# Kernel optimization log

Measured on AMD Instinct MI355X. Metric: run time of the kernel, lower is better.

The kernel has to match this reference:

```python
import jax, jax.numpy as jnp
import numpy as np

N, L, E, CE = 16384, 50, 64, 128
N_USERS, N_RATINGS, N_CONTENTS = 100000, 6, 50000

def _lin(key, din, dout):
    k1, k2 = jax.random.split(key)
    s = 1.0 / np.sqrt(din)
    return (jax.random.uniform(k1, (din, dout), jnp.float32, -s, s),
            jax.random.uniform(k2, (dout,), jnp.float32, -s, s))

def setup_inputs() -> dict:
    key = jax.random.key(0)
    ks = jax.random.split(key, 16)
    We_w, We_b = _lin(ks[0], CE, E)
    W1_w, W1_b = _lin(ks[1], 2 * E, E)
    W2_w, W2_b = _lin(ks[2], E, E)
    A1_w, A1_b = _lin(ks[3], 2 * E, E)
    A2_w, A2_b = _lin(ks[4], E, E)
    A3_w, A3_b = _lin(ks[5], E, 1)
    Ow_w, Ow_b = _lin(ks[6], 2 * E, E)
    return {
        "u2e": jax.random.normal(ks[7], (N_USERS, E), jnp.float32),
        "r2e": jax.random.normal(ks[8], (N_RATINGS, E), jnp.float32),
        "content_emb": jax.random.normal(ks[9], (N_CONTENTS, CE), jnp.float32),
        "We_w": We_w, "We_b": We_b,
        "W1_w": W1_w, "W1_b": W1_b,
        "W2_w": W2_w, "W2_b": W2_b,
        "A1_w": A1_w, "A1_b": A1_b,
        "A2_w": A2_w, "A2_b": A2_b,
        "A3_w": A3_w, "A3_b": A3_b,
        "Ow_w": Ow_w, "Ow_b": Ow_b,
        "nodes": jnp.arange(N, dtype=jnp.int64) if jax.config.jax_enable_x64 else jnp.arange(N, dtype=jnp.int32),
        "pu_history": jax.random.randint(ks[10], (N, L), 0, N_USERS),
        "pr_history": jax.random.randint(ks[11], (N, L), 0, N_RATINGS),
        "lengths": jax.random.randint(ks[12], (N,), 1, L + 1),
        "pr_content": jax.random.randint(ks[13], (N,), 0, N_CONTENTS),
    }

def reference(u2e, r2e, content_emb, We_w, We_b, W1_w, W1_b, W2_w, W2_b,
              A1_w, A1_b, A2_w, A2_b, A3_w, A3_b, Ow_w, Ow_b,
              nodes, pu_history, pr_history, lengths, pr_content):
    # mask of valid (non-padded) neighbors per node: [N, L]
    mask = jnp.arange(pu_history.shape[1])[None, :] < lengths[:, None]
    # post content representation: [N, E]
    post = jax.nn.relu(content_emb[pr_content] @ We_w + We_b)
    # neighbor embeddings: [N, L, E]
    u = u2e[pu_history]
    r = r2e[pr_history]
    x = jax.nn.relu(jnp.concatenate([u, r], axis=-1) @ W1_w + W1_b)
    o = jax.nn.relu(x @ W2_w + W2_b)  # [N, L, E]
    # attention over variable-length neighbor history
    pr = jnp.broadcast_to(post[:, None, :], o.shape)
    a = jax.nn.relu(jnp.concatenate([o, pr], axis=-1) @ A1_w + A1_b)
    a = jax.nn.relu(a @ A2_w + A2_b)
    logits = (a @ A3_w + A3_b)[..., 0]  # [N, L]
    logits = jnp.where(mask, logits, -jnp.inf)
    att = jax.nn.softmax(logits, axis=1)  # [N, L], padded slots -> 0
    hist = jnp.einsum("nl,nle->ne", att, o)  # [N, E]
    out = jax.nn.relu(jnp.concatenate([hist, post], axis=-1) @ Ow_w + Ow_b)
    return out
```

## Files before the change

### kernel.cpp

```cpp
#include <hip/hip_runtime.h>
#include <hip/hip_bf16.h>
#include <math.h>


#define NN 16384
#define LL 50
#define EE 64
#define NUE 6400000

typedef __attribute__((ext_vector_type(8))) short short8;
typedef __attribute__((ext_vector_type(4))) float f32x4;

static __device__ __forceinline__ unsigned short f2bf(float x) {
  __hip_bfloat16 h = __float2bfloat16(x);
  unsigned short u;
  __builtin_memcpy(&u, &h, 2);
  return u;
}

static __device__ __forceinline__ float bf2f(unsigned short u) {
  unsigned int v = ((unsigned int)u) << 16;
  float f;
  __builtin_memcpy(&f, &v, 4);
  return f;
}

static __device__ __forceinline__ f32x4 ld4(const float* p) {
  return *(const f32x4*)p;
}

static __device__ __forceinline__ f32x4 relu4(f32x4 a) {
  f32x4 r;
  r[0] = fmaxf(a[0], 0.f); r[1] = fmaxf(a[1], 0.f);
  r[2] = fmaxf(a[2], 0.f); r[3] = fmaxf(a[3], 0.f);
  return r;
}

static __device__ __forceinline__ void gl_lds16(const unsigned short* g,
                                                unsigned char* l) {
  __builtin_amdgcn_global_load_lds(
      (const __attribute__((address_space(1))) void*)g,
      (__attribute__((address_space(3))) void*)l, 16, 0, 0);
}

#define MFMA(A, B, C) __builtin_amdgcn_mfma_f32_16x16x32_bf16((A), (B), (C), 0, 0, 0)
#define SWZ(row, byteoff) ((byteoff) ^ (((row) & 7) << 4))

__global__ __launch_bounds__(256)
void conv_kernel(const float* __restrict__ u2e, const float* __restrict__ r2e,
                 unsigned short* __restrict__ ur_bf) {
  const int total8 = (NUE + 384) / 8;
  for (int i = blockIdx.x * 256 + (int)threadIdx.x; i < total8;
       i += gridDim.x * 256) {
    const long long e0 = (long long)i * 8;
    const float* src = (e0 < NUE) ? (u2e + e0) : (r2e + (e0 - NUE));
    float4 a = *(const float4*)src;
    float4 b = *(const float4*)(src + 4);
    short8 v;
    v[0] = (short)f2bf(a.x); v[1] = (short)f2bf(a.y);
    v[2] = (short)f2bf(a.z); v[3] = (short)f2bf(a.w);
    v[4] = (short)f2bf(b.x); v[5] = (short)f2bf(b.y);
    v[6] = (short)f2bf(b.z); v[7] = (short)f2bf(b.w);
    *reinterpret_cast<short8*>(ur_bf + e0) = v;
  }
}

__global__ __launch_bounds__(256)
void setup_kernel(const float* __restrict__ content_emb,
                  const int* __restrict__ pr_content,
                  const float* __restrict__ We_w, const float* __restrict__ We_b,
                  const float* __restrict__ A1_w, const float* __restrict__ A1_b,
                  float* __restrict__ post_ws, float* __restrict__ abase_ws) {
  const int sub = (int)threadIdx.x >> 6;
  const int e = (int)threadIdx.x & 63;
  const int n = blockIdx.x * 4 + sub;
  __shared__ float ce_s[4][128];
  __shared__ float post_s[4][64];
  const float* ce = content_emb + (size_t)pr_content[n] * 128;
  ce_s[sub][e] = ce[e];
  ce_s[sub][64 + e] = ce[64 + e];
  __syncthreads();
  float acc = We_b[e];
#pragma unroll 8
  for (int k = 0; k < 128; ++k) acc = fmaf(ce_s[sub][k], We_w[k * EE + e], acc);
  float po = fmaxf(acc, 0.f);
  post_s[sub][e] = po;
  post_ws[(size_t)n * EE + e] = po;
  __syncthreads();
  float ab = A1_b[e];
#pragma unroll 8
  for (int k = 0; k < 64; ++k)
    ab = fmaf(post_s[sub][k], A1_w[(64 + k) * EE + e], ab);
  abase_ws[(size_t)n * EE + e] = ab;
}

__global__ __launch_bounds__(1024)
void aux_kernel(const int* __restrict__ lengths,
                const float* __restrict__ W1_w, const float* __restrict__ W2_w,
                const float* __restrict__ A1_w, const float* __restrict__ A2_w,
                int* __restrict__ buckets, int* __restrict__ wdesc,
                int* __restrict__ Wout, unsigned short* __restrict__ frag_ws) {
  const int tid = (int)threadIdx.x;
  const int lanei = tid & 63;
  __shared__ int cnt_s[4];
  if (tid < 4) cnt_s[tid] = 0;
  __syncthreads();

  for (int i0 = 0; i0 < NN; i0 += 1024) {
    const int n = i0 + tid;
    const int nt = (lengths[n] + 15) >> 4;
#pragma unroll
    for (int b = 1; b <= 4; ++b) {
      const unsigned long long mask = __ballot(nt == b);
      if (mask) {
        const int leader = __ffsll((long long)mask) - 1;
        int base = 0;
        if (lanei == leader) base = atomicAdd(&cnt_s[b - 1], (int)__popcll(mask));
        base = __shfl(base, leader);
        if (nt == b) {
          const int rank = __popcll(mask & ((1ull << lanei) - 1ull));
          buckets[(b - 1) * NN + base + rank] = n;
        }
      }
    }
  }
  __syncthreads();

  const int c1 = cnt_s[0], c2 = cnt_s[1], c3 = cnt_s[2], c4 = cnt_s[3];
  const int u1 = (c1 < c3) ? c1 : c3;
  const int p2 = c2 >> 1, odd2 = c2 & 1;
  const int rem1 = c1 - u1;
  const int o2ones = odd2 ? ((rem1 < 2) ? rem1 : 2) : 0;
  const int rem1b = rem1 - o2ones;
  const int w4 = c4, w3 = c3, w2 = p2 + odd2, w1 = (rem1b + 3) >> 2;
  const int W = w4 + w3 + w2 + w1;
  if (tid == 0) *Wout = W;

  const int* b1 = buckets;
  const int* b2 = buckets + NN;
  const int* b3 = buckets + 2 * NN;
  const int* b4 = buckets + 3 * NN;
#define ENC(n, t) ((n) | ((t) << 14) | (lengths[(n)] << 16))
  for (int w = tid; w < W; w += 1024) {
    int d0 = -1, d1 = -1, d2 = -1, d3 = -1;
    if (w < w4) {
      const int n = b4[w];
      d0 = ENC(n, 0); d1 = ENC(n, 1); d2 = ENC(n, 2); d3 = ENC(n, 3);
    } else if (w < w4 + w3) {
      const int i = w - w4;
      const int n = b3[i];
      d0 = ENC(n, 0); d1 = ENC(n, 1); d2 = ENC(n, 2);
      if (i < u1) d3 = ENC(b1[i], 0);
    } else if (w < w4 + w3 + w2) {
      const int i = w - w4 - w3;
      if (i < p2) {
        const int a = b2[2 * i], b = b2[2 * i + 1];
        d0 = ENC(a, 0); d1 = ENC(a, 1); d2 = ENC(b, 0); d3 = ENC(b, 1);
      } else {
        const int a = b2[c2 - 1];
        d0 = ENC(a, 0); d1 = ENC(a, 1);
        if (o2ones > 0) d2 = ENC(b1[u1], 0);
        if (o2ones > 1) d3 = ENC(b1[u1 + 1], 0);
      }
    } else {
      const int i = w - w4 - w3 - w2;
      const int basei = u1 + o2ones + 4 * i;
      if (basei + 0 < c1) d0 = ENC(b1[basei + 0], 0);
      if (basei + 1 < c1) d1 = ENC(b1[basei + 1], 0);
      if (basei + 2 < c1) d2 = ENC(b1[basei + 2], 0);
      if (basei + 3 < c1) d3 = ENC(b1[basei + 3], 0);
    }
    int4 v; v.x = d0; v.y = d1; v.z = d2; v.w = d3;
    *(int4*)(wdesc + 4 * w) = v;
  }
#undef ENC

  for (int idx = tid; idx < 2560; idx += 1024) {
    const float* Wm;
    int w, s, lane;
    if (idx < 1024) {
      w = idx >> 8; s = (idx >> 6) & 3; lane = idx & 63; Wm = W1_w;
    } else {
      int r = idx - 1024;
      int li = r >> 9;
      w = (r >> 7) & 3; s = (r >> 6) & 1; lane = r & 63;
      Wm = (li == 0) ? W2_w : (li == 1) ? A1_w : A2_w;
    }
    const int g = lane >> 4, c = lane & 15;
#pragma unroll
    for (int j = 0; j < 8; ++j)
      frag_ws[idx * 8 + j] = f2bf(Wm[(32 * s + 8 * g + j) * EE + 16 * w + c]);
  }
}

__global__
__attribute__((amdgpu_flat_work_group_size(256, 256)))
__attribute__((amdgpu_waves_per_eu(4, 4)))
void fused_kernel(const unsigned short* __restrict__ ur_bf,
                  const float* __restrict__ W1_b, const float* __restrict__ W2_b,
                  const float* __restrict__ A2_b,
                  const float* __restrict__ A3_w, const float* __restrict__ A3_b,
                  const float* __restrict__ Ow_w, const float* __restrict__ Ow_b,
                  const int* __restrict__ pu_history,
                  const int* __restrict__ pr_history,
                  const short8* __restrict__ pf,
                  const float* __restrict__ post_ws,
                  const float* __restrict__ abase_ws,
                  const int* __restrict__ wdesc, const int* __restrict__ Wptr,
                  float* __restrict__ out) {
  const int tid = (int)threadIdx.x;
  const int lane = tid & 63;
  const int w = tid >> 6;
  const int g = lane >> 4;
  const int c = lane & 15;

  __shared__ __align__(16) unsigned char xb0[16384];
  __shared__ __align__(16) unsigned char xb1[8192];
  __shared__ __align__(16) unsigned char xb2[8192];
  __shared__ float bias_s[256];
  __shared__ float lpart[4][64];
  __shared__ float att_s[64];
  __shared__ float h_s[4][128];

  short8 Wf1[4], Wf2[2], Wf3[2], Wf4[2];
#pragma unroll
  for (int s = 0; s < 4; ++s) Wf1[s] = pf[(w * 4 + s) * 64 + lane];
#pragma unroll
  for (int s = 0; s < 2; ++s) {
    Wf2[s] = pf[1024 + (w * 2 + s) * 64 + lane];
    Wf3[s] = pf[1536 + (w * 2 + s) * 64 + lane];
    Wf4[s] = pf[2048 + (w * 2 + s) * 64 + lane];
  }
  if (tid < 64) {
    bias_s[tid]       = W1_b[tid];
    bias_s[64 + tid]  = W2_b[tid];
    bias_s[128 + tid] = A2_b[tid];
    bias_s[192 + tid] = A3_w[tid];
  }

  const float b3 = A3_b[0];
  const float owb = Ow_b[lane];
  const unsigned short* rbase = ur_bf + NUE;
  const int Wtot = *Wptr;
  const int stride = gridDim.x;

  const int r0 = lane >> 4;
  const int cE = (lane & 15) ^ r0;
  const int cO = (lane & 15) ^ (r0 + 4);
  const unsigned short* tabE = ((cE < 8) ? ur_bf : rbase) + (cE & 7) * 8;
  const unsigned short* tabO = ((cO < 8) ? ur_bf : rbase) + (cO & 7) * 8;
  const int* histE = (cE < 8) ? pu_history : pr_history;
  const int* histO = (cO < 8) ? pu_history : pr_history;
  unsigned char* const sbase = xb0 + w * 4096;

  {
    const int dn = wdesc[blockIdx.x * 4 + w];
    if (dn >= 0) {
      const int nd = (dn & 0x3FFF) * LL + (((dn >> 14) & 3) << 4);
      const int ln = (dn >> 16) & 63;
      const int lim = ln - (((dn >> 14) & 3) << 4);
#pragma unroll
      for (int b = 0; b < 4; ++b) {
        const int row = b * 4 + r0;
        const bool vv = row < lim;
        const int* hh = (b & 1) ? histO : histE;
        const unsigned short* tt = (b & 1) ? tabO : tabE;
        if (vv) {
          const int idx = hh[nd + row];
          gl_lds16(tt + (size_t)idx * EE, sbase + b * 1024);
        }
      }
    }
  }
  __syncthreads();

  for (int wi = blockIdx.x; wi < Wtot; wi += stride) {
    const int d0 = wdesc[wi * 4 + 0];
    const int d1 = wdesc[wi * 4 + 1];
    const int d2 = wdesc[wi * 4 + 2];
    const int d3 = wdesc[wi * 4 + 3];

    const int win = wi + stride;
    int sidx0 = 0, sidx1 = 0, sidx2 = 0, sidx3 = 0;
    int svmask = 0;
    if (win < Wtot) {
      const int dn = wdesc[win * 4 + w];
      if (dn >= 0) {
        const int nd = (dn & 0x3FFF) * LL + (((dn >> 14) & 3) << 4);
        const int lim = ((dn >> 16) & 63) - (((dn >> 14) & 3) << 4);
        if (r0 + 0  < lim) { sidx0 = histE[nd + r0];      svmask |= 1; }
        if (r0 + 4  < lim) { sidx1 = histO[nd + r0 + 4];  svmask |= 2; }
        if (r0 + 8  < lim) { sidx2 = histE[nd + r0 + 8];  svmask |= 4; }
        if (r0 + 12 < lim) { sidx3 = histO[nd + r0 + 12]; svmask |= 8; }
      }
    }

    f32x4 acc[4];

    {
      const f32x4 binit = ld4(bias_s + 16 * w + 4 * g);
#pragma unroll
      for (int rt = 0; rt < 4; ++rt) acc[rt] = binit;
#pragma unroll
      for (int s = 0; s < 4; ++s)
#pragma unroll
        for (int rt = 0; rt < 4; ++rt) {
          const int row = rt * 16 + c;
          const short8 bf =
              *(const short8*)(xb0 + SWZ(row, row * 256 + s * 64 + g * 16));
          acc[rt] = MFMA(Wf1[s], bf, acc[rt]);
        }
#pragma unroll
      for (int rt = 0; rt < 4; ++rt) {
        const f32x4 v = relu4(acc[rt]);
        ushort4 p;
        p.x = f2bf(v[0]); p.y = f2bf(v[1]); p.z = f2bf(v[2]); p.w = f2bf(v[3]);
        const int row = rt * 16 + c;
        *(ushort4*)(xb1 + SWZ(row, row * 128 + w * 32 + g * 8)) = p;
      }
    }
    __syncthreads();

    if (svmask & 1) gl_lds16(tabE + (size_t)sidx0 * EE, sbase);
    if (svmask & 2) gl_lds16(tabO + (size_t)sidx1 * EE, sbase + 1024);
    if (svmask & 4) gl_lds16(tabE + (size_t)sidx2 * EE, sbase + 2048);
    if (svmask & 8) gl_lds16(tabO + (size_t)sidx3 * EE, sbase + 3072);

    {
      const f32x4 binit = ld4(bias_s + 64 + 16 * w + 4 * g);
#pragma unroll
      for (int rt = 0; rt < 4; ++rt) acc[rt] = binit;
#pragma unroll
      for (int s = 0; s < 2; ++s)
#pragma unroll
        for (int rt = 0; rt < 4; ++rt) {
          const int row = rt * 16 + c;
          const short8 bf =
              *(const short8*)(xb1 + SWZ(row, row * 128 + s * 64 + g * 16));
          acc[rt] = MFMA(Wf2[s], bf, acc[rt]);
        }
#pragma unroll
      for (int rt = 0; rt < 4; ++rt) {
        const f32x4 v = relu4(acc[rt]);
        ushort4 p;
        p.x = f2bf(v[0]); p.y = f2bf(v[1]); p.z = f2bf(v[2]); p.w = f2bf(v[3]);
        const int row = rt * 16 + c;
        *(ushort4*)(xb2 + SWZ(row, row * 128 + w * 32 + g * 8)) = p;
      }
    }
    __syncthreads();

    {
      {
        const int n0 = (d0 >= 0) ? (d0 & 0x3FFF) : 0;
        const int n1 = (d1 >= 0) ? (d1 & 0x3FFF) : 0;
        const int n2 = (d2 >= 0) ? (d2 & 0x3FFF) : 0;
        const int n3 = (d3 >= 0) ? (d3 & 0x3FFF) : 0;
        acc[0] = ld4(abase_ws + (size_t)n0 * EE + 16 * w + 4 * g);
        acc[1] = ld4(abase_ws + (size_t)n1 * EE + 16 * w + 4 * g);
        acc[2] = ld4(abase_ws + (size_t)n2 * EE + 16 * w + 4 * g);
        acc[3] = ld4(abase_ws + (size_t)n3 * EE + 16 * w + 4 * g);
      }
#pragma unroll
      for (int s = 0; s < 2; ++s)
#pragma unroll
        for (int rt = 0; rt < 4; ++rt) {
          const int row = rt * 16 + c;
          const short8 bf =
              *(const short8*)(xb2 + SWZ(row, row * 128 + s * 64 + g * 16));
          acc[rt] = MFMA(Wf3[s], bf, acc[rt]);
        }
#pragma unroll
      for (int rt = 0; rt < 4; ++rt) {
        const f32x4 v = relu4(acc[rt]);
        ushort4 p;
        p.x = f2bf(v[0]); p.y = f2bf(v[1]); p.z = f2bf(v[2]); p.w = f2bf(v[3]);
        const int row = rt * 16 + c;
        *(ushort4*)(xb1 + SWZ(row, row * 128 + w * 32 + g * 8)) = p;
      }
    }
    __syncthreads();

    {
      const f32x4 binit = ld4(bias_s + 128 + 16 * w + 4 * g);
#pragma unroll
      for (int rt = 0; rt < 4; ++rt) acc[rt] = binit;
#pragma unroll
      for (int s = 0; s < 2; ++s)
#pragma unroll
        for (int rt = 0; rt < 4; ++rt) {
          const int row = rt * 16 + c;
          const short8 bf =
              *(const short8*)(xb1 + SWZ(row, row * 128 + s * 64 + g * 16));
          acc[rt] = MFMA(Wf4[s], bf, acc[rt]);
        }
      const f32x4 a3 = ld4(bias_s + 192 + 16 * w + 4 * g);
#pragma unroll
      for (int rt = 0; rt < 4; ++rt) {
        const f32x4 r = relu4(acc[rt]);
        float p = r[0] * a3[0];
        p = fmaf(r[1], a3[1], p);
        p = fmaf(r[2], a3[2], p);
        p = fmaf(r[3], a3[3], p);
        p += __shfl_xor(p, 16);
        p += __shfl_xor(p, 32);
        if (lane < 16) lpart[w][rt * 16 + lane] = p;
      }
    }
    __syncthreads();

    {
      const int dw = (w == 0) ? d0 : (w == 1) ? d1 : (w == 2) ? d2 : d3;
      if (dw >= 0 && ((dw >> 14) & 3) == 0) {
        const int fnode = dw & 0x3FFF;
        const int flen = (dw >> 16) & 63;
        const bool vr = (lane < flen);
        float lg = -INFINITY;
        if (vr) {
          const int row = w * 16 + lane;
          lg = lpart[0][row] + lpart[1][row] + lpart[2][row] + lpart[3][row] + b3;
        }
        float mx = lg;
#pragma unroll
        for (int off = 32; off > 0; off >>= 1)
          mx = fmaxf(mx, __shfl_xor(mx, off));
        const float e = __expf(lg - mx);
        float sm = e;
#pragma unroll
        for (int off = 32; off > 0; off >>= 1) sm += __shfl_xor(sm, off);
        if (vr) att_s[w * 16 + lane] = e / sm;

        float h0 = 0.f, h1 = 0.f;
        for (int r2 = 0; r2 + 1 < flen; r2 += 2) {
          const int ra = w * 16 + r2, rb = ra + 1;
          const unsigned short oa =
              *(const unsigned short*)(xb2 + SWZ(ra, ra * 128 + lane * 2));
          const unsigned short ob =
              *(const unsigned short*)(xb2 + SWZ(rb, rb * 128 + lane * 2));
          h0 = fmaf(att_s[ra], bf2f(oa), h0);
          h1 = fmaf(att_s[rb], bf2f(ob), h1);
        }
        if (flen & 1) {
          const int ra = w * 16 + flen - 1;
          const unsigned short oa =
              *(const unsigned short*)(xb2 + SWZ(ra, ra * 128 + lane * 2));
          h0 = fmaf(att_s[ra], bf2f(oa), h0);
        }
        h_s[w][lane] = h0 + h1;
        h_s[w][64 + lane] = post_ws[(size_t)fnode * EE + lane];

        float s0 = 0.f, s1 = 0.f, s2 = 0.f, s3 = 0.f;
#pragma unroll 8
        for (int k = 0; k < 128; k += 4) {
          s0 = fmaf(h_s[w][k],     Ow_w[(k)     * EE + lane], s0);
          s1 = fmaf(h_s[w][k + 1], Ow_w[(k + 1) * EE + lane], s1);
          s2 = fmaf(h_s[w][k + 2], Ow_w[(k + 2) * EE + lane], s2);
          s3 = fmaf(h_s[w][k + 3], Ow_w[(k + 3) * EE + lane], s3);
        }
        const float a = owb + ((s0 + s1) + (s2 + s3));
        out[(size_t)fnode * EE + lane] = fmaxf(a, 0.f);
      }
    }
  }
}

template <int K>
__device__ __forceinline__ void mm2(const float* row0, const float* row1,
                                    const float* __restrict__ W, int e,
                                    float& acc0, float& acc1) {
  const float4* r0 = (const float4*)row0;
  const float4* r1 = (const float4*)row1;
#pragma unroll 4
  for (int k4 = 0; k4 < K / 4; ++k4) {
    float4 va = r0[k4];
    float4 vb = r1[k4];
    const float* w = W + (k4 * 4) * EE + e;
    float w0 = w[0], w1 = w[EE], w2 = w[2 * EE], w3 = w[3 * EE];
    acc0 = fmaf(va.x, w0, acc0);  acc1 = fmaf(vb.x, w0, acc1);
    acc0 = fmaf(va.y, w1, acc0);  acc1 = fmaf(vb.y, w1, acc1);
    acc0 = fmaf(va.z, w2, acc0);  acc1 = fmaf(vb.z, w2, acc1);
    acc0 = fmaf(va.w, w3, acc0);  acc1 = fmaf(vb.w, w3, acc1);
  }
}

__global__ __launch_bounds__(256, 4)
void postenc_kernel(
    const float* __restrict__ u2e, const float* __restrict__ r2e,
    const float* __restrict__ content_emb,
    const float* __restrict__ We_w, const float* __restrict__ We_b,
    const float* __restrict__ W1_w, const float* __restrict__ W1_b,
    const float* __restrict__ W2_w, const float* __restrict__ W2_b,
    const float* __restrict__ A1_w, const float* __restrict__ A1_b,
    const float* __restrict__ A2_w, const float* __restrict__ A2_b,
    const float* __restrict__ A3_w, const float* __restrict__ A3_b,
    const float* __restrict__ Ow_w, const float* __restrict__ Ow_b,
    const int* __restrict__ pu_history, const int* __restrict__ pr_history,
    const int* __restrict__ lengths, const int* __restrict__ pr_content,
    float* __restrict__ out) {
  const int n = blockIdx.x;
  const int tid = (int)threadIdx.x;
  const int e = tid & 63;
  const int g = tid >> 6;

  __shared__ float post_s[EE];
  __shared__ float abase_s[EE];
  __shared__ float in_s[8][128];
  __shared__ float x_s[8][EE];
  __shared__ float a_s[8][EE];
  __shared__ float o_s[56][EE];
  __shared__ float logit_s[EE];
  __shared__ float att_s[EE];
  __shared__ float red_s[4][EE];

  const int len = lengths[n];
  float p = 0.f;

  if (g == 0) {
    const float* ce = content_emb + (size_t)pr_content[n] * 128;
    float acc = We_b[e];
#pragma unroll 4
    for (int k = 0; k < 128; ++k) acc = fmaf(ce[k], We_w[k * EE + e], acc);
    p = fmaxf(acc, 0.f);
    post_s[e] = p;
    float ab = A1_b[e];
#pragma unroll
    for (int k = 0; k < 64; ++k) {
      float pk = __shfl(p, k);
      ab = fmaf(pk, A1_w[(64 + k) * EE + e], ab);
    }
    abase_s[e] = ab;
    logit_s[e] = -INFINITY;
  }
  __syncthreads();

  for (int lb = 0; lb < 56; lb += 8) {
    const int l0 = lb + g;
    const int l1 = l0 + 4;
    const bool v0 = l0 < LL;
    const bool v1 = l1 < LL;

    int pu0 = 0, pr0 = 0, pu1 = 0, pr1 = 0;
    if (v0) { pu0 = pu_history[n * LL + l0]; pr0 = pr_history[n * LL + l0]; }
    if (v1) { pu1 = pu_history[n * LL + l1]; pr1 = pr_history[n * LL + l1]; }
    in_s[g][e]          = v0 ? u2e[(size_t)pu0 * EE + e] : 0.f;
    in_s[g][64 + e]     = v0 ? r2e[pr0 * EE + e]         : 0.f;
    in_s[g + 4][e]      = v1 ? u2e[(size_t)pu1 * EE + e] : 0.f;
    in_s[g + 4][64 + e] = v1 ? r2e[pr1 * EE + e]         : 0.f;
    __syncthreads();

    float acc0 = W1_b[e], acc1 = acc0;
    mm2<128>(in_s[g], in_s[g + 4], W1_w, e, acc0, acc1);
    x_s[g][e]     = fmaxf(acc0, 0.f);
    x_s[g + 4][e] = fmaxf(acc1, 0.f);
    __syncthreads();

    acc0 = W2_b[e]; acc1 = acc0;
    mm2<64>(x_s[g], x_s[g + 4], W2_w, e, acc0, acc1);
    float o0 = fmaxf(acc0, 0.f);
    float o1 = fmaxf(acc1, 0.f);
    if (v0) o_s[l0][e] = o0;
    if (v1) o_s[l1][e] = o1;
    x_s[g][e]     = o0;
    x_s[g + 4][e] = o1;
    __syncthreads();

    acc0 = abase_s[e]; acc1 = acc0;
    mm2<64>(x_s[g], x_s[g + 4], A1_w, e, acc0, acc1);
    a_s[g][e]     = fmaxf(acc0, 0.f);
    a_s[g + 4][e] = fmaxf(acc1, 0.f);
    __syncthreads();

    acc0 = A2_b[e]; acc1 = acc0;
    mm2<64>(a_s[g], a_s[g + 4], A2_w, e, acc0, acc1);
    float w3 = A3_w[e];
    float p0 = fmaxf(acc0, 0.f) * w3;
    float p1 = fmaxf(acc1, 0.f) * w3;
#pragma unroll
    for (int off = 32; off > 0; off >>= 1) {
      p0 += __shfl_xor(p0, off);
      p1 += __shfl_xor(p1, off);
    }
    if (e == 0) {
      float b3 = A3_b[0];
      if (l0 < len) logit_s[l0] = p0 + b3;
      if (l1 < len) logit_s[l1] = p1 + b3;
    }
    __syncthreads();
  }

  if (g == 0) {
    float lg = logit_s[e];
    float m = lg;
#pragma unroll
    for (int off = 32; off > 0; off >>= 1) m = fmaxf(m, __shfl_xor(m, off));
    float pe = __expf(lg - m);
    float sm = pe;
#pragma unroll
    for (int off = 32; off > 0; off >>= 1) sm += __shfl_xor(sm, off);
    att_s[e] = pe / sm;
  }
  __syncthreads();

  {
    const int l_lo = 13 * g;
    const int l_hi = (13 * g + 13 < LL) ? 13 * g + 13 : LL;
    float h = 0.f;
    for (int l = l_lo; l < l_hi; ++l) h = fmaf(att_s[l], o_s[l][e], h);
    red_s[g][e] = h;
  }
  __syncthreads();

  if (g == 0) {
    float h = red_s[0][e] + red_s[1][e] + red_s[2][e] + red_s[3][e];
    float acc = Ow_b[e];
#pragma unroll
    for (int k = 0; k < 64; ++k) {
      float hk = __shfl(h, k);
      acc = fmaf(hk, Ow_w[k * EE + e], acc);
    }
#pragma unroll
    for (int k = 0; k < 64; ++k) {
      float pk = __shfl(p, k);
      acc = fmaf(pk, Ow_w[(64 + k) * EE + e], acc);
    }
    out[(size_t)n * EE + e] = fmaxf(acc, 0.f);
  }
}

extern "C" void kernel_launch(void* const* d_in, const int* in_sizes, int n_in,
                              void* d_out, int out_size, void* d_ws, size_t ws_size,
                              hipStream_t stream) {
  const float* u2e         = (const float*)d_in[0];
  const float* r2e         = (const float*)d_in[1];
  const float* content_emb = (const float*)d_in[2];
  const float* We_w = (const float*)d_in[3];
  const float* We_b = (const float*)d_in[4];
  const float* W1_w = (const float*)d_in[5];
  const float* W1_b = (const float*)d_in[6];
  const float* W2_w = (const float*)d_in[7];
  const float* W2_b = (const float*)d_in[8];
  const float* A1_w = (const float*)d_in[9];
  const float* A1_b = (const float*)d_in[10];
  const float* A2_w = (const float*)d_in[11];
  const float* A2_b = (const float*)d_in[12];
  const float* A3_w = (const float*)d_in[13];
  const float* A3_b = (const float*)d_in[14];
  const float* Ow_w = (const float*)d_in[15];
  const float* Ow_b = (const float*)d_in[16];
  const int* pu_history = (const int*)d_in[18];
  const int* pr_history = (const int*)d_in[19];
  const int* lengths    = (const int*)d_in[20];
  const int* pr_content = (const int*)d_in[21];
  float* out = (float*)d_out;

  const size_t FR_OFF  = 0;
  const size_t PO_OFF  = 65536;
  const size_t AB_OFF  = PO_OFF + (size_t)NN * EE * 4;
  const size_t UBF_OFF = AB_OFF + (size_t)NN * EE * 4;
  const size_t CNT_OFF = UBF_OFF + (size_t)(NUE + 384) * 2;
  const size_t BK_OFF  = CNT_OFF + 256;
  const size_t WD_OFF  = BK_OFF + (size_t)4 * NN * 4;
  const size_t NEED    = WD_OFF + (size_t)NN * 4 * 4;

  if (ws_size < NEED) {
    postenc_kernel<<<NN, 256, 0, stream>>>(
        u2e, r2e, content_emb, We_w, We_b, W1_w, W1_b, W2_w, W2_b,
        A1_w, A1_b, A2_w, A2_b, A3_w, A3_b, Ow_w, Ow_b,
        pu_history, pr_history, lengths, pr_content, out);
    return;
  }

  char* wsp = (char*)d_ws;
  unsigned short* frag_ws = (unsigned short*)(wsp + FR_OFF);
  float* post_ws  = (float*)(wsp + PO_OFF);
  float* abase_ws = (float*)(wsp + AB_OFF);
  unsigned short* ur_bf = (unsigned short*)(wsp + UBF_OFF);
  int* Wout_ws = (int*)(wsp + CNT_OFF);
  int* bk_ws   = (int*)(wsp + BK_OFF);
  int* wd_ws   = (int*)(wsp + WD_OFF);

  conv_kernel<<<2048, 256, 0, stream>>>(u2e, r2e, ur_bf);
  aux_kernel<<<1, 1024, 0, stream>>>(lengths, W1_w, W2_w, A1_w, A2_w,
                                     bk_ws, wd_ws, Wout_ws, frag_ws);
  setup_kernel<<<NN / 4, 256, 0, stream>>>(content_emb, pr_content, We_w, We_b,
                                           A1_w, A1_b, post_ws, abase_ws);
  fused_kernel<<<1024, 256, 0, stream>>>(
      ur_bf, W1_b, W2_b, A2_b, A3_w, A3_b, Ow_w, Ow_b,
      pu_history, pr_history, (const short8*)frag_ws,
      post_ws, abase_ws, wd_ws, Wout_ws, out);
}
```

Before: 160.2 us.

## Merge preprocessing kernels into one launch and stage per-node vectors via LDS

Folds the conversion, setup, bucketing and weight-fragment kernels into a single block-indexed pre_kernel, so several small launches and their serialisation gaps go away. The bucketing still runs in one block, now with 256 threads instead of 1024, which could lengthen that serial tail. The fused kernel's grid doubles to 2048 blocks and gains a guard for blocks past the work count. It now loads the per-node abase and post vectors into LDS with async global_load_lds early in each iteration instead of gathering them from global later.

```diff
diff --git a/kernel.cpp b/kernel.cpp
--- a/kernel.cpp
+++ b/kernel.cpp
@@ -42,154 +42,160 @@
       (const __attribute__((address_space(1))) void*)g,
       (__attribute__((address_space(3))) void*)l, 16, 0, 0);
 }
+static __device__ __forceinline__ void gl_lds4(const float* g, float* l) {
+  __builtin_amdgcn_global_load_lds(
+      (const __attribute__((address_space(1))) void*)g,
+      (__attribute__((address_space(3))) void*)l, 4, 0, 0);
+}
 
 #define MFMA(A, B, C) __builtin_amdgcn_mfma_f32_16x16x32_bf16((A), (B), (C), 0, 0, 0)
 #define SWZ(row, byteoff) ((byteoff) ^ (((row) & 7) << 4))
 
 __global__ __launch_bounds__(256)
-void conv_kernel(const float* __restrict__ u2e, const float* __restrict__ r2e,
-                 unsigned short* __restrict__ ur_bf) {
-  const int total8 = (NUE + 384) / 8;
-  for (int i = blockIdx.x * 256 + (int)threadIdx.x; i < total8;
-       i += gridDim.x * 256) {
-    const long long e0 = (long long)i * 8;
-    const float* src = (e0 < NUE) ? (u2e + e0) : (r2e + (e0 - NUE));
-    float4 a = *(const float4*)src;
-    float4 b = *(const float4*)(src + 4);
-    short8 v;
-    v[0] = (short)f2bf(a.x); v[1] = (short)f2bf(a.y);
-    v[2] = (short)f2bf(a.z); v[3] = (short)f2bf(a.w);
-    v[4] = (short)f2bf(b.x); v[5] = (short)f2bf(b.y);
-    v[6] = (short)f2bf(b.z); v[7] = (short)f2bf(b.w);
-    *reinterpret_cast<short8*>(ur_bf + e0) = v;
-  }
-}
-
-__global__ __launch_bounds__(256)
-void setup_kernel(const float* __restrict__ content_emb,
-                  const int* __restrict__ pr_content,
-                  const float* __restrict__ We_w, const float* __restrict__ We_b,
-                  const float* __restrict__ A1_w, const float* __restrict__ A1_b,
-                  float* __restrict__ post_ws, float* __restrict__ abase_ws) {
-  const int sub = (int)threadIdx.x >> 6;
-  const int e = (int)threadIdx.x & 63;
-  const int n = blockIdx.x * 4 + sub;
+void pre_kernel(const float* __restrict__ u2e, const float* __restrict__ r2e,
+                const float* __restrict__ content_emb,
+                const int* __restrict__ pr_content,
+                const float* __restrict__ We_w, const float* __restrict__ We_b,
+                const float* __restrict__ W1_w, const float* __restrict__ W2_w,
+                const float* __restrict__ A1_w, const float* __restrict__ A1_b,
+                const float* __restrict__ A2_w,
+                const int* __restrict__ lengths,
+                unsigned short* __restrict__ ur_bf,
+                int* __restrict__ buckets, int* __restrict__ wdesc,
+                int* __restrict__ Wout, unsigned short* __restrict__ frag_ws,
+                float* __restrict__ post_ws, float* __restrict__ abase_ws) {
+  const int b = blockIdx.x;
+  const int tid = (int)threadIdx.x;
   __shared__ float ce_s[4][128];
   __shared__ float post_s[4][64];
-  const float* ce = content_emb + (size_t)pr_content[n] * 128;
-  ce_s[sub][e] = ce[e];
-  ce_s[sub][64 + e] = ce[64 + e];
-  __syncthreads();
-  float acc = We_b[e];
+  __shared__ int cnt_s[4];
+
+  if (b < 2048) {
+    const int total8 = (NUE + 384) / 8;
+    for (int i = b * 256 + tid; i < total8; i += 2048 * 256) {
+      const long long e0 = (long long)i * 8;
+      const float* src = (e0 < NUE) ? (u2e + e0) : (r2e + (e0 - NUE));
+      float4 a = *(const float4*)src;
+      float4 bb = *(const float4*)(src + 4);
+      short8 v;
+      v[0] = (short)f2bf(a.x); v[1] = (short)f2bf(a.y);
+      v[2] = (short)f2bf(a.z); v[3] = (short)f2bf(a.w);
+      v[4] = (short)f2bf(bb.x); v[5] = (short)f2bf(bb.y);
+      v[6] = (short)f2bf(bb.z); v[7] = (short)f2bf(bb.w);
+      *reinterpret_cast<short8*>(ur_bf + e0) = v;
+    }
+  } else if (b < 6144) {
+    const int sub = tid >> 6;
+    const int e = tid & 63;
+    const int n = (b - 2048) * 4 + sub;
+    const float* ce = content_emb + (size_t)pr_content[n] * 128;
+    ce_s[sub][e] = ce[e];
+    ce_s[sub][64 + e] = ce[64 + e];
+    __syncthreads();
+    float acc = We_b[e];
 #pragma unroll 8
-  for (int k = 0; k < 128; ++k) acc = fmaf(ce_s[sub][k], We_w[k * EE + e], acc);
-  float po = fmaxf(acc, 0.f);
-  post_s[sub][e] = po;
-  post_ws[(size_t)n * EE + e] = po;
-  __syncthreads();
-  float ab = A1_b[e];
+    for (int k = 0; k < 128; ++k)
+      acc = fmaf(ce_s[sub][k], We_w[k * EE + e], acc);
+    float po = fmaxf(acc, 0.f);
+    post_s[sub][e] = po;
+    post_ws[(size_t)n * EE + e] = po;
+    __syncthreads();
+    float ab = A1_b[e];
 #pragma unroll 8
-  for (int k = 0; k < 64; ++k)
-    ab = fmaf(post_s[sub][k], A1_w[(64 + k) * EE + e], ab);
-  abase_ws[(size_t)n * EE + e] = ab;
-}
-
-__global__ __launch_bounds__(1024)
-void aux_kernel(const int* __restrict__ lengths,
-                const float* __restrict__ W1_w, const float* __restrict__ W2_w,
-                const float* __restrict__ A1_w, const float* __restrict__ A2_w,
-                int* __restrict__ buckets, int* __restrict__ wdesc,
-                int* __restrict__ Wout, unsigned short* __restrict__ frag_ws) {
-  const int tid = (int)threadIdx.x;
-  const int lanei = tid & 63;
-  __shared__ int cnt_s[4];
-  if (tid < 4) cnt_s[tid] = 0;
-  __syncthreads();
-
-  for (int i0 = 0; i0 < NN; i0 += 1024) {
-    const int n = i0 + tid;
-    const int nt = (lengths[n] + 15) >> 4;
-#pragma unroll
-    for (int b = 1; b <= 4; ++b) {
-      const unsigned long long mask = __ballot(nt == b);
-      if (mask) {
-        const int leader = __ffsll((long long)mask) - 1;
-        int base = 0;
-        if (lanei == leader) base = atomicAdd(&cnt_s[b - 1], (int)__popcll(mask));
-        base = __shfl(base, leader);
-        if (nt == b) {
-          const int rank = __popcll(mask & ((1ull << lanei) - 1ull));
-          buckets[(b - 1) * NN + base + rank] = n;
+    for (int k = 0; k < 64; ++k)
+      ab = fmaf(post_s[sub][k], A1_w[(64 + k) * EE + e], ab);
+    abase_ws[(size_t)n * EE + e] = ab;
+  } else if (b == 6144) {
+    const int lanei = tid & 63;
+    if (tid < 4) cnt_s[tid] = 0;
+    __syncthreads();
+    for (int i0 = 0; i0 < NN; i0 += 256) {
+      const int n = i0 + tid;
+      const int nt = (lengths[n] + 15) >> 4;
+#pragma unroll
+      for (int bb = 1; bb <= 4; ++bb) {
+        const unsigned long long mask = __ballot(nt == bb);
+        if (mask) {
+          const int leader = __ffsll((long long)mask) - 1;
+          int base = 0;
+          if (lanei == leader)
+            base = atomicAdd(&cnt_s[bb - 1], (int)__popcll(mask));
+          base = __shfl(base, leader);
+          if (nt == bb) {
+            const int rank = __popcll(mask & ((1ull << lanei) - 1ull));
+            buckets[(bb - 1) * NN + base + rank] = n;
+          }
         }
       }
     }
-  }
-  __syncthreads();
-
-  const int c1 = cnt_s[0], c2 = cnt_s[1], c3 = cnt_s[2], c4 = cnt_s[3];
-  const int u1 = (c1 < c3) ? c1 : c3;
-  const int p2 = c2 >> 1, odd2 = c2 & 1;
-  const int rem1 = c1 - u1;
-  const int o2ones = odd2 ? ((rem1 < 2) ? rem1 : 2) : 0;
-  const int rem1b = rem1 - o2ones;
-  const int w4 = c4, w3 = c3, w2 = p2 + odd2, w1 = (rem1b + 3) >> 2;
-  const int W = w4 + w3 + w2 + w1;
-  if (tid == 0) *Wout = W;
-
-  const int* b1 = buckets;
-  const int* b2 = buckets + NN;
-  const int* b3 = buckets + 2 * NN;
-  const int* b4 = buckets + 3 * NN;
+    __syncthreads();
+
+    const int c1 = cnt_s[0], c2 = cnt_s[1], c3 = cnt_s[2], c4 = cnt_s[3];
+    const int u1 = (c1 < c3) ? c1 : c3;
+    const int p2 = c2 >> 1, odd2 = c2 & 1;
+    const int rem1 = c1 - u1;
+    const int o2ones = odd2 ? ((rem1 < 2) ? rem1 : 2) : 0;
+    const int rem1b = rem1 - o2ones;
+    const int w4 = c4, w3 = c3, w2 = p2 + odd2, w1 = (rem1b + 3) >> 2;
+    const int W = w4 + w3 + w2 + w1;
+    if (tid == 0) *Wout = W;
+
+    const int* b1 = buckets;
+    const int* b2 = buckets + NN;
+    const int* b3 = buckets + 2 * NN;
+    const int* b4 = buckets + 3 * NN;
 #define ENC(n, t) ((n) | ((t) << 14) | (lengths[(n)] << 16))
-  for (int w = tid; w < W; w += 1024) {
-    int d0 = -1, d1 = -1, d2 = -1, d3 = -1;
-    if (w < w4) {
-      const int n = b4[w];
-      d0 = ENC(n, 0); d1 = ENC(n, 1); d2 = ENC(n, 2); d3 = ENC(n, 3);
-    } else if (w < w4 + w3) {
-      const int i = w - w4;
-      const int n = b3[i];
-      d0 = ENC(n, 0); d1 = ENC(n, 1); d2 = ENC(n, 2);
-      if (i < u1) d3 = ENC(b1[i], 0);
-    } else if (w < w4 + w3 + w2) {
-      const int i = w - w4 - w3;
-      if (i < p2) {
-        const int a = b2[2 * i], b = b2[2 * i + 1];
-        d0 = ENC(a, 0); d1 = ENC(a, 1); d2 = ENC(b, 0); d3 = ENC(b, 1);
+    for (int w = tid; w < W; w += 256) {
+      int d0 = -1, d1 = -1, d2 = -1, d3 = -1;
+      if (w < w4) {
+        const int n = b4[w];
+        d0 = ENC(n, 0); d1 = ENC(n, 1); d2 = ENC(n, 2); d3 = ENC(n, 3);
+      } else if (w < w4 + w3) {
+        const int i = w - w4;
+        const int n = b3[i];
+        d0 = ENC(n, 0); d1 = ENC(n, 1); d2 = ENC(n, 2);
+        if (i < u1) d3 = ENC(b1[i], 0);
+      } else if (w < w4 + w3 + w2) {
+        const int i = w - w4 - w3;
+        if (i < p2) {
+          const int a = b2[2 * i], bbn = b2[2 * i + 1];
+          d0 = ENC(a, 0); d1 = ENC(a, 1); d2 = ENC(bbn, 0); d3 = ENC(bbn, 1);
+        } else {
+          const int a = b2[c2 - 1];
+          d0 = ENC(a, 0); d1 = ENC(a, 1);
+          if (o2ones > 0) d2 = ENC(b1[u1], 0);
+          if (o2ones > 1) d3 = ENC(b1[u1 + 1], 0);
+        }
       } else {
-        const int a = b2[c2 - 1];
-        d0 = ENC(a, 0); d1 = ENC(a, 1);
-        if (o2ones > 0) d2 = ENC(b1[u1], 0);
-        if (o2ones > 1) d3 = ENC(b1[u1 + 1], 0);
-      }
-    } else {
-      const int i = w - w4 - w3 - w2;
-      const int basei = u1 + o2ones + 4 * i;
-      if (basei + 0 < c1) d0 = ENC(b1[basei + 0], 0);
-      if (basei + 1 < c1) d1 = ENC(b1[basei + 1], 0);
-      if (basei + 2 < c1) d2 = ENC(b1[basei + 2], 0);
-      if (basei + 3 < c1) d3 = ENC(b1[basei + 3], 0);
-    }
-    int4 v; v.x = d0; v.y = d1; v.z = d2; v.w = d3;
-    *(int4*)(wdesc + 4 * w) = v;
-  }
+        const int i = w - w4 - w3 - w2;
+        const int basei = u1 + o2ones + 4 * i;
+        if (basei + 0 < c1) d0 = ENC(b1[basei + 0], 0);
+        if (basei + 1 < c1) d1 = ENC(b1[basei + 1], 0);
+        if (basei + 2 < c1) d2 = ENC(b1[basei + 2], 0);
+        if (basei + 3 < c1) d3 = ENC(b1[basei + 3], 0);
+      }
+      int4 v; v.x = d0; v.y = d1; v.z = d2; v.w = d3;
+      *(int4*)(wdesc + 4 * w) = v;
+    }
 #undef ENC
-
-  for (int idx = tid; idx < 2560; idx += 1024) {
-    const float* Wm;
-    int w, s, lane;
-    if (idx < 1024) {
-      w = idx >> 8; s = (idx >> 6) & 3; lane = idx & 63; Wm = W1_w;
-    } else {
-      int r = idx - 1024;
-      int li = r >> 9;
-      w = (r >> 7) & 3; s = (r >> 6) & 1; lane = r & 63;
-      Wm = (li == 0) ? W2_w : (li == 1) ? A1_w : A2_w;
-    }
-    const int g = lane >> 4, c = lane & 15;
-#pragma unroll
-    for (int j = 0; j < 8; ++j)
-      frag_ws[idx * 8 + j] = f2bf(Wm[(32 * s + 8 * g + j) * EE + 16 * w + c]);
+  } else {
+    const int idx = (b - 6145) * 256 + tid;
+    if (idx < 2560) {
+      const float* Wm;
+      int w, s, lane;
+      if (idx < 1024) {
+        w = idx >> 8; s = (idx >> 6) & 3; lane = idx & 63; Wm = W1_w;
+      } else {
+        int r = idx - 1024;
+        int li = r >> 9;
+        w = (r >> 7) & 3; s = (r >> 6) & 1; lane = r & 63;
+        Wm = (li == 0) ? W2_w : (li == 1) ? A1_w : A2_w;
+      }
+      const int g = lane >> 4, c = lane & 15;
+#pragma unroll
+      for (int j = 0; j < 8; ++j)
+        frag_ws[idx * 8 + j] = f2bf(Wm[(32 * s + 8 * g + j) * EE + 16 * w + c]);
+    }
   }
 }
 
@@ -221,6 +227,8 @@
   __shared__ float lpart[4][64];
   __shared__ float att_s[64];
   __shared__ float h_s[4][128];
+  __shared__ float ab_s[4][64];
+  __shared__ float po_s[4][64];
 
   short8 Wf1[4], Wf2[2], Wf3[2], Wf4[2];
 #pragma unroll
@@ -253,19 +261,17 @@
   const int* histO = (cO < 8) ? pu_history : pr_history;
   unsigned char* const sbase = xb0 + w * 4096;
 
-  {
+  if (blockIdx.x < Wtot) {
     const int dn = wdesc[blockIdx.x * 4 + w];
     if (dn >= 0) {
       const int nd = (dn & 0x3FFF) * LL + (((dn >> 14) & 3) << 4);
-      const int ln = (dn >> 16) & 63;
-      const int lim = ln - (((dn >> 14) & 3) << 4);
+      const int lim = ((dn >> 16) & 63) - (((dn >> 14) & 3) << 4);
 #pragma unroll
       for (int b = 0; b < 4; ++b) {
         const int row = b * 4 + r0;
-        const bool vv = row < lim;
         const int* hh = (b & 1) ? histO : histE;
         const unsigned short* tt = (b & 1) ? tabO : tabE;
-        if (vv) {
+        if (row < lim) {
           const int idx = hh[nd + row];
           gl_lds16(tt + (size_t)idx * EE, sbase + b * 1024);
         }
@@ -275,10 +281,17 @@
   __syncthreads();
 
   for (int wi = blockIdx.x; wi < Wtot; wi += stride) {
-    const int d0 = wdesc[wi * 4 + 0];
-    const int d1 = wdesc[wi * 4 + 1];
-    const int d2 = wdesc[wi * 4 + 2];
-    const int d3 = wdesc[wi * 4 + 3];
+    const int4 dd = *(const int4*)(wdesc + wi * 4);
+    const int d0 = dd.x, d1 = dd.y, d2 = dd.z, d3 = dd.w;
+    const int dw = (w == 0) ? d0 : (w == 1) ? d1 : (w == 2) ? d2 : d3;
+    const bool fin = (dw >= 0) && (((dw >> 14) & 3) == 0);
+    const int fnode = dw & 0x3FFF;
+    const int flen = (dw >> 16) & 63;
+
+    if (dw >= 0) {
+      gl_lds4(abase_ws + (size_t)fnode * EE + lane, ab_s[w]);
+      gl_lds4(post_ws + (size_t)fnode * EE + lane, po_s[w]);
+    }
 
     const int win = wi + stride;
     int sidx0 = 0, sidx1 = 0, sidx2 = 0, sidx3 = 0;
@@ -351,16 +364,9 @@
     __syncthreads();
 
     {
-      {
-        const int n0 = (d0 >= 0) ? (d0 & 0x3FFF) : 0;
-        const int n1 = (d1 >= 0) ? (d1 & 0x3FFF) : 0;
-        const int n2 = (d2 >= 0) ? (d2 & 0x3FFF) : 0;
-        const int n3 = (d3 >= 0) ? (d3 & 0x3FFF) : 0;
-        acc[0] = ld4(abase_ws + (size_t)n0 * EE + 16 * w + 4 * g);
-        acc[1] = ld4(abase_ws + (size_t)n1 * EE + 16 * w + 4 * g);
-        acc[2] = ld4(abase_ws + (size_t)n2 * EE + 16 * w + 4 * g);
-        acc[3] = ld4(abase_ws + (size_t)n3 * EE + 16 * w + 4 * g);
-      }
+#pragma unroll
+      for (int rt = 0; rt < 4; ++rt)
+        acc[rt] = ld4(&ab_s[rt][16 * w + 4 * g]);
 #pragma unroll
       for (int s = 0; s < 2; ++s)
 #pragma unroll
@@ -409,57 +415,52 @@
     }
     __syncthreads();
 
-    {
-      const int dw = (w == 0) ? d0 : (w == 1) ? d1 : (w == 2) ? d2 : d3;
-      if (dw >= 0 && ((dw >> 14) & 3) == 0) {
-        const int fnode = dw & 0x3FFF;
-        const int flen = (dw >> 16) & 63;
-        const bool vr = (lane < flen);
-        float lg = -INFINITY;
-        if (vr) {
-          const int row = w * 16 + lane;
-          lg = lpart[0][row] + lpart[1][row] + lpart[2][row] + lpart[3][row] + b3;
-        }
-        float mx = lg;
-#pragma unroll
-        for (int off = 32; off > 0; off >>= 1)
-          mx = fmaxf(mx, __shfl_xor(mx, off));
-        const float e = __expf(lg - mx);
-        float sm = e;
-#pragma unroll
-        for (int off = 32; off > 0; off >>= 1) sm += __shfl_xor(sm, off);
-        if (vr) att_s[w * 16 + lane] = e / sm;
-
-        float h0 = 0.f, h1 = 0.f;
-        for (int r2 = 0; r2 + 1 < flen; r2 += 2) {
-          const int ra = w * 16 + r2, rb = ra + 1;
-          const unsigned short oa =
-              *(const unsigned short*)(xb2 + SWZ(ra, ra * 128 + lane * 2));
-          const unsigned short ob =
-              *(const unsigned short*)(xb2 + SWZ(rb, rb * 128 + lane * 2));
-          h0 = fmaf(att_s[ra], bf2f(oa), h0);
-          h1 = fmaf(att_s[rb], bf2f(ob), h1);
-        }
-        if (flen & 1) {
-          const int ra = w * 16 + flen - 1;
-          const unsigned short oa =
-              *(const unsigned short*)(xb2 + SWZ(ra, ra * 128 + lane * 2));
-          h0 = fmaf(att_s[ra], bf2f(oa), h0);
-        }
-        h_s[w][lane] = h0 + h1;
-        h_s[w][64 + lane] = post_ws[(size_t)fnode * EE + lane];
-
-        float s0 = 0.f, s1 = 0.f, s2 = 0.f, s3 = 0.f;
+    if (fin) {
+      const bool vr = (lane < flen);
+      float lg = -INFINITY;
+      if (vr) {
+        const int row = w * 16 + lane;
+        lg = lpart[0][row] + lpart[1][row] + lpart[2][row] + lpart[3][row] + b3;
+      }
+      float mx = lg;
+#pragma unroll
+      for (int off = 32; off > 0; off >>= 1)
+        mx = fmaxf(mx, __shfl_xor(mx, off));
+      const float e = __expf(lg - mx);
+      float sm = e;
+#pragma unroll
+      for (int off = 32; off > 0; off >>= 1) sm += __shfl_xor(sm, off);
+      if (vr) att_s[w * 16 + lane] = e / sm;
+
+      float h0 = 0.f, h1 = 0.f;
+      for (int r2 = 0; r2 + 1 < flen; r2 += 2) {
+        const int ra = w * 16 + r2, rb = ra + 1;
+        const unsigned short oa =
+            *(const unsigned short*)(xb2 + SWZ(ra, ra * 128 + lane * 2));
+        const unsigned short ob =
+            *(const unsigned short*)(xb2 + SWZ(rb, rb * 128 + lane * 2));
+        h0 = fmaf(att_s[ra], bf2f(oa), h0);
+        h1 = fmaf(att_s[rb], bf2f(ob), h1);
+      }
+      if (flen & 1) {
+        const int ra = w * 16 + flen - 1;
+        const unsigned short oa =
+            *(const unsigned short*)(xb2 + SWZ(ra, ra * 128 + lane * 2));
+        h0 = fmaf(att_s[ra], bf2f(oa), h0);
+      }
+      h_s[w][lane] = h0 + h1;
+      h_s[w][64 + lane] = po_s[w][lane];
+
+      float s0 = 0.f, s1 = 0.f, s2 = 0.f, s3 = 0.f;
 #pragma unroll 8
-        for (int k = 0; k < 128; k += 4) {
-          s0 = fmaf(h_s[w][k],     Ow_w[(k)     * EE + lane], s0);
-          s1 = fmaf(h_s[w][k + 1], Ow_w[(k + 1) * EE + lane], s1);
-          s2 = fmaf(h_s[w][k + 2], Ow_w[(k + 2) * EE + lane], s2);
-          s3 = fmaf(h_s[w][k + 3], Ow_w[(k + 3) * EE + lane], s3);
-        }
-        const float a = owb + ((s0 + s1) + (s2 + s3));
-        out[(size_t)fnode * EE + lane] = fmaxf(a, 0.f);
-      }
+      for (int k = 0; k < 128; k += 4) {
+        s0 = fmaf(h_s[w][k],     Ow_w[(k)     * EE + lane], s0);
+        s1 = fmaf(h_s[w][k + 1], Ow_w[(k + 1) * EE + lane], s1);
+        s2 = fmaf(h_s[w][k + 2], Ow_w[(k + 2) * EE + lane], s2);
+        s3 = fmaf(h_s[w][k + 3], Ow_w[(k + 3) * EE + lane], s3);
+      }
+      const float a = owb + ((s0 + s1) + (s2 + s3));
+      out[(size_t)fnode * EE + lane] = fmaxf(a, 0.f);
     }
   }
 }
@@ -679,12 +680,11 @@
   int* bk_ws   = (int*)(wsp + BK_OFF);
   int* wd_ws   = (int*)(wsp + WD_OFF);
 
-  conv_kernel<<<2048, 256, 0, stream>>>(u2e, r2e, ur_bf);
-  aux_kernel<<<1, 1024, 0, stream>>>(lengths, W1_w, W2_w, A1_w, A2_w,
-                                     bk_ws, wd_ws, Wout_ws, frag_ws);
-  setup_kernel<<<NN / 4, 256, 0, stream>>>(content_emb, pr_content, We_w, We_b,
-                                           A1_w, A1_b, post_ws, abase_ws);
-  fused_kernel<<<1024, 256, 0, stream>>>(
+  pre_kernel<<<6155, 256, 0, stream>>>(
+      u2e, r2e, content_emb, pr_content, We_w, We_b, W1_w, W2_w,
+      A1_w, A1_b, A2_w, lengths, ur_bf, bk_ws, wd_ws, Wout_ws,
+      frag_ws, post_ws, abase_ws);
+  fused_kernel<<<2048, 256, 0, stream>>>(
       ur_bf, W1_b, W2_b, A2_b, A3_w, A3_b, Ow_w, Ow_b,
       pu_history, pr_history, (const short8*)frag_ws,
       post_ws, abase_ws, wd_ws, Wout_ws, out);
```

After: 214.3 us. +33.8%, slower.
